# Kernel optimization log

Measured on AMD Instinct MI355X. Metric: run time of the kernel, lower is better.

The kernel has to match this reference:

```python
import jax, jax.numpy as jnp
import numpy as np

TSHAPE = (256, 256, 1024)
RANK = 32


def setup_inputs() -> dict:
    key = jax.random.key(0)
    k0, k1, k2 = jax.random.split(key, 3)
    # Nonnegative factor matrices, columns normalized to sum to 1 (as in NTF.__init__
    # via reinit_mode + norm_mode_within_factor).
    W0 = jax.random.uniform(k0, (TSHAPE[0], RANK), dtype=jnp.float32)
    W1 = jax.random.uniform(k1, (TSHAPE[1], RANK), dtype=jnp.float32)
    W2 = jax.random.uniform(k2, (TSHAPE[2], RANK), dtype=jnp.float32)
    W0 = W0 / W0.sum(axis=0)
    W1 = W1 / W1.sum(axis=0)
    W2 = W2 / W2.sum(axis=0)
    return {"W0": W0, "W1": W1, "W2": W2}


def reference(W0, W1, W2):
    # CP reconstruction: outer_prod(modes).sum(axis=-1)
    # == sum_r W0[:, r] (x) W1[:, r] (x) W2[:, r]  -> shape TSHAPE
    # einsum fuses the rank reduction, avoiding the (i, j, k, r) intermediate.
    return jnp.einsum("ir,jr,kr->ijk", W0, W1, W2)
```

## Files before the change

kernel.cpp:

```cpp
#include <hip/hip_runtime.h>


constexpr int I_DIM  = 256;
constexpr int J_DIM  = 256;
constexpr int K_DIM  = 1024;
constexpr int RNK    = 32;
constexpr int JSEG   = 64;
constexpr int KSPLIT = 2;
constexpr int KCHUNK = K_DIM / KSPLIT;

typedef float f32x2 __attribute__((ext_vector_type(2)));

__global__ void transpose_w2(const float* __restrict__ W2, float* __restrict__ W2T) {
    int idx = blockIdx.x * 256 + threadIdx.x;
    int r = idx >> 10;
    int k = idx & (K_DIM - 1);
    W2T[r * K_DIM + k] = W2[k * RNK + r];
}

__global__ void precompute_c(const float* __restrict__ W0, const float* __restrict__ W1,
                             float* __restrict__ C) {
    int idx = blockIdx.x * 256 + threadIdx.x;
    int r = idx & 31;
    int j = (idx >> 5) & 255;
    int i = idx >> 13;
    C[idx] = W0[i * RNK + r] * W1[j * RNK + r];
}

__global__ __launch_bounds__(256, 6) void cp_recon_f2(const float* __restrict__ C,
                                                      const float* __restrict__ W2T,
                                                      float* __restrict__ out) {
    const int b     = blockIdx.x;
    const int khalf = b & (KSPLIT - 1);
    const int jseg  = (b >> 1) & 3;
    const int i     = b >> 3;
    const int jbase = jseg * JSEG;
    const int k     = khalf * KCHUNK + threadIdx.x * 2;

    float2 w[RNK];
#pragma unroll
    for (int r = 0; r < RNK; ++r)
        w[r] = *reinterpret_cast<const float2*>(&W2T[r * K_DIM + k]);

    const float* __restrict__ crow = C + (size_t)(i * J_DIM + jbase) * RNK;
    float* __restrict__ obase = out + (size_t)(i * J_DIM + jbase) * K_DIM + k;

#pragma unroll 2
    for (int jj = 0; jj < JSEG; ++jj) {
        const float* __restrict__ cj = crow + jj * RNK;
        float ax = 0.f, ay = 0.f;
#pragma unroll
        for (int r = 0; r < RNK; ++r) {
            float s = cj[r];
            ax = fmaf(s, w[r].x, ax);
            ay = fmaf(s, w[r].y, ay);
        }
        f32x2 t = { ax, ay };
        *reinterpret_cast<f32x2*>(obase + (size_t)jj * K_DIM) = t;
    }
}

constexpr int JT = 8;
__global__ __launch_bounds__(256, 4) void cp_recon_d(const float* __restrict__ W0,
                                                     const float* __restrict__ W1,
                                                     const float* __restrict__ W2,
                                                     float* __restrict__ out) {
    __shared__ __align__(16) float c[JT][RNK];
    const int i     = blockIdx.x >> 5;
    const int jbase = (blockIdx.x & 31) * JT;
    const int tid   = threadIdx.x;

    if (tid < JT * RNK) {
        int jj = tid >> 5;
        int r  = tid & 31;
        c[jj][r] = W0[i * RNK + r] * W1[(jbase + jj) * RNK + r];
    }
    __syncthreads();

    const int k = tid * 4;
    float4 acc[JT];
#pragma unroll
    for (int jj = 0; jj < JT; ++jj) acc[jj] = make_float4(0.f, 0.f, 0.f, 0.f);

    for (int rc = 0; rc < RNK; rc += 4) {
        float4 row[4];
#pragma unroll
        for (int q = 0; q < 4; ++q)
            row[q] = *reinterpret_cast<const float4*>(&W2[(k + q) * RNK + rc]);
#pragma unroll
        for (int jj = 0; jj < JT; ++jj) {
            float4 c4 = *reinterpret_cast<const float4*>(&c[jj][rc]);
            acc[jj].x = fmaf(c4.x, row[0].x, fmaf(c4.y, row[0].y, fmaf(c4.z, row[0].z, fmaf(c4.w, row[0].w, acc[jj].x))));
            acc[jj].y = fmaf(c4.x, row[1].x, fmaf(c4.y, row[1].y, fmaf(c4.z, row[1].z, fmaf(c4.w, row[1].w, acc[jj].y))));
            acc[jj].z = fmaf(c4.x, row[2].x, fmaf(c4.y, row[2].y, fmaf(c4.z, row[2].z, fmaf(c4.w, row[2].w, acc[jj].z))));
            acc[jj].w = fmaf(c4.x, row[3].x, fmaf(c4.y, row[3].y, fmaf(c4.z, row[3].z, fmaf(c4.w, row[3].w, acc[jj].w))));
        }
    }
#pragma unroll
    for (int jj = 0; jj < JT; ++jj) {
        int o = (i * J_DIM + jbase + jj) * K_DIM + k;
        *reinterpret_cast<float4*>(&out[o]) = acc[jj];
    }
}

extern "C" void kernel_launch(void* const* d_in, const int* in_sizes, int n_in,
                              void* d_out, int out_size, void* d_ws, size_t ws_size,
                              hipStream_t stream) {
    const float* W0 = (const float*)d_in[0];
    const float* W1 = (const float*)d_in[1];
    const float* W2 = (const float*)d_in[2];
    float* out = (float*)d_out;

    const size_t w2t_bytes = (size_t)RNK * K_DIM * sizeof(float);
    const size_t c_bytes   = (size_t)I_DIM * J_DIM * RNK * sizeof(float);

    if (ws_size >= w2t_bytes + c_bytes) {
        float* W2T  = (float*)d_ws;
        float* Cbuf = (float*)((char*)d_ws + w2t_bytes);
        transpose_w2<<<(RNK * K_DIM) / 256, 256, 0, stream>>>(W2, W2T);
        precompute_c<<<(I_DIM * J_DIM * RNK) / 256, 256, 0, stream>>>(W0, W1, Cbuf);
        const int grid = I_DIM * (J_DIM / JSEG) * KSPLIT;
        cp_recon_f2<<<grid, 256, 0, stream>>>(Cbuf, W2T, out);
    } else {
        cp_recon_d<<<I_DIM * (J_DIM / JT), 256, 0, stream>>>(W0, W1, W2, out);
    }
}
```

Measured before the change: 73.64 us.

## Widen main kernel to float4 per thread covering full K, halve j segment

The main reconstruction kernel now gives each thread four consecutive k values across the whole K dimension instead of two values in a split half, and cuts the j segment per block from 64 to 32. Each scalar C load now feeds four FMAs, and stores become 16-byte vectors, which reduces load and issue overhead per output. In exchange, per-thread register use for the W2 tile doubles to 128 floats, so launch bounds drop to 3 blocks per CU and occupancy may fall.

```diff
diff --git a/kernel.cpp b/kernel.cpp
--- a/kernel.cpp
+++ b/kernel.cpp
@@ -5,11 +5,9 @@
 constexpr int J_DIM  = 256;
 constexpr int K_DIM  = 1024;
 constexpr int RNK    = 32;
-constexpr int JSEG   = 64;
-constexpr int KSPLIT = 2;
-constexpr int KCHUNK = K_DIM / KSPLIT;
+constexpr int JSEG   = 32;
 
-typedef float f32x2 __attribute__((ext_vector_type(2)));
+typedef float f32x4 __attribute__((ext_vector_type(4)));
 
 __global__ void transpose_w2(const float* __restrict__ W2, float* __restrict__ W2T) {
     int idx = blockIdx.x * 256 + threadIdx.x;
@@ -27,20 +25,19 @@
     C[idx] = W0[i * RNK + r] * W1[j * RNK + r];
 }
 
-__global__ __launch_bounds__(256, 6) void cp_recon_f2(const float* __restrict__ C,
-                                                      const float* __restrict__ W2T,
-                                                      float* __restrict__ out) {
+__global__ __launch_bounds__(256, 3) void cp_recon_f4s(const float* __restrict__ C,
+                                                       const float* __restrict__ W2T,
+                                                       float* __restrict__ out) {
     const int b     = blockIdx.x;
-    const int khalf = b & (KSPLIT - 1);
-    const int jseg  = (b >> 1) & 3;
+    const int jseg  = b & 7;
     const int i     = b >> 3;
     const int jbase = jseg * JSEG;
-    const int k     = khalf * KCHUNK + threadIdx.x * 2;
+    const int k     = threadIdx.x * 4;
 
-    float2 w[RNK];
+    float4 w[RNK];
 #pragma unroll
     for (int r = 0; r < RNK; ++r)
-        w[r] = *reinterpret_cast<const float2*>(&W2T[r * K_DIM + k]);
+        w[r] = *reinterpret_cast<const float4*>(&W2T[r * K_DIM + k]);
 
     const float* __restrict__ crow = C + (size_t)(i * J_DIM + jbase) * RNK;
     float* __restrict__ obase = out + (size_t)(i * J_DIM + jbase) * K_DIM + k;
@@ -48,15 +45,17 @@
 #pragma unroll 2
     for (int jj = 0; jj < JSEG; ++jj) {
         const float* __restrict__ cj = crow + jj * RNK;
-        float ax = 0.f, ay = 0.f;
+        float4 acc = make_float4(0.f, 0.f, 0.f, 0.f);
 #pragma unroll
         for (int r = 0; r < RNK; ++r) {
             float s = cj[r];
-            ax = fmaf(s, w[r].x, ax);
-            ay = fmaf(s, w[r].y, ay);
+            acc.x = fmaf(s, w[r].x, acc.x);
+            acc.y = fmaf(s, w[r].y, acc.y);
+            acc.z = fmaf(s, w[r].z, acc.z);
+            acc.w = fmaf(s, w[r].w, acc.w);
         }
-        f32x2 t = { ax, ay };
-        *reinterpret_cast<f32x2*>(obase + (size_t)jj * K_DIM) = t;
+        f32x4 t = { acc.x, acc.y, acc.z, acc.w };
+        *reinterpret_cast<f32x4*>(obase + (size_t)jj * K_DIM) = t;
     }
 }
 
@@ -119,8 +118,8 @@
         float* Cbuf = (float*)((char*)d_ws + w2t_bytes);
         transpose_w2<<<(RNK * K_DIM) / 256, 256, 0, stream>>>(W2, W2T);
         precompute_c<<<(I_DIM * J_DIM * RNK) / 256, 256, 0, stream>>>(W0, W1, Cbuf);
-        const int grid = I_DIM * (J_DIM / JSEG) * KSPLIT;
-        cp_recon_f2<<<grid, 256, 0, stream>>>(Cbuf, W2T, out);
+        const int grid = I_DIM * (J_DIM / JSEG);
+        cp_recon_f4s<<<grid, 256, 0, stream>>>(Cbuf, W2T, out);
     } else {
         cp_recon_d<<<I_DIM * (J_DIM / JT), 256, 0, stream>>>(W0, W1, W2, out);
     }
```

After: 67.52 us. -8.3%, faster.
